# Optimization experiments

Hardware: AMD Instinct MI355X
Metric: run time of the kernel (lower is better)

## Reference

```python
import jax, jax.numpy as jnp
import numpy as np

B, NF, NI = 4, 8, 1
C_ASPP = 512
H32, W32 = 32, 32
H8, W8 = 128, 128
C = C_ASPP // 16  # 32 channels after PixelShuffle(4)
D = 32 * 4 + 4 * 1 + 4 + 1  # 137 dynamic-kernel params per instance
BN_EPS = 1e-5


def pixel_shuffle(x, r):
    # torch PixelShuffle: out[n, c, h*r+i, w*r+j] = in[n, c*r*r + i*r + j, h, w]
    n, cr2, h, w = x.shape
    c = cr2 // (r * r)
    x = x.reshape(n, c, r, r, h, w)
    x = x.transpose(0, 1, 4, 2, 5, 3)
    return x.reshape(n, c, h * r, w * r)


def conv2d(x, w, b, pad):
    y = jax.lax.conv_general_dilated(
        x, w, window_strides=(1, 1), padding=[(pad, pad), (pad, pad)],
        dimension_numbers=("NCHW", "OIHW", "NCHW"))
    return y + b[None, :, None, None]


def setup_inputs() -> dict:
    key = jax.random.key(0)
    ks = jax.random.split(key, 6)
    return {
        "embedding": jax.random.normal(ks[0], (B * NF, C_ASPP, H32, W32), jnp.float32),
        "inc_kernels": jax.random.normal(ks[1], (B, NF, NI, D), jnp.float32) * 0.1,
        "coarse_masks": jax.random.uniform(ks[2], (B, NF, NI, H8, W8), dtype=jnp.float32),
        "conv_w": jax.random.normal(ks[3], (C, C, 3, 3), jnp.float32) * 0.05,
        "conv_b": jnp.zeros((C,), jnp.float32),
        "bn_gamma": jnp.ones((C,), jnp.float32),
        "bn_beta": jnp.zeros((C,), jnp.float32),
        "bn_mean": jnp.zeros((C,), jnp.float32),
        "bn_var": jnp.ones((C,), jnp.float32),
        "smooth_w": jax.random.normal(ks[4], (1, 2, 5, 5), jnp.float32) * 0.05,
        "smooth_b": jnp.zeros((1,), jnp.float32),
    }


def reference(embedding, inc_kernels, coarse_masks, conv_w, conv_b,
              bn_gamma, bn_beta, bn_mean, bn_var, smooth_w, smooth_b):
    # inc_conv: PixelShuffle(4) -> Conv3x3 -> BatchNorm(eval) -> ReLU
    x = pixel_shuffle(embedding, 4)              # (B*NF, 32, 128, 128)
    x = conv2d(x, conv_w, conv_b, 1)
    scale = (bn_gamma / jnp.sqrt(bn_var + BN_EPS))[None, :, None, None]
    x = (x - bn_mean[None, :, None, None]) * scale + bn_beta[None, :, None, None]
    x = jax.nn.relu(x)

    # per-instance dynamic 1x1 convs (groups = B*NF*NI; NI=1 so each frame is a group)
    G = B * NF * NI
    k = inc_kernels.reshape(G, D)
    w1 = k[:, :128].reshape(G, 4, 32)            # layer1: 32 -> 4
    w2 = k[:, 128:132].reshape(G, 1, 4)          # layer2: 4 -> 1
    b1 = k[:, 132:136]
    b2 = k[:, 136:137]

    hfeat = jax.nn.relu(jnp.einsum('goc,gchw->gohw', w1, x) + b1[:, :, None, None])
    y = jnp.einsum('goc,gchw->gohw', w2, hfeat) + b2[:, :, None, None]  # (G,1,H8,W8)

    m = coarse_masks.reshape(G, 1, H8, W8)
    z = jnp.concatenate([jax.nn.sigmoid(y), m], axis=1)  # (G, 2, H8, W8)
    z = conv2d(z, smooth_w, smooth_b, 2)                 # inc_smooth 5x5
    return z.reshape(B * NF, NI, H8, W8)
```

## Files before the change

kernel.cpp:

```cpp
#include <hip/hip_runtime.h>


typedef __attribute__((ext_vector_type(8))) short short8;
typedef __attribute__((ext_vector_type(4))) float f32x4;

static __device__ __forceinline__ ushort f2bf(float x) {
    union { float f; uint u; } v; v.f = x;
    uint r = v.u + 0x7fffu + ((v.u >> 16) & 1u);
    return (ushort)(r >> 16);
}
static __device__ __forceinline__ float bf2f(ushort u) {
    union { uint u; float f; } v; v.u = ((uint)u) << 16; return v.f;
}

#define SIG_ELEMS (32 * 128 * 128)
#define BFRAG_OFF (SIG_ELEMS * 4)
#define SC_OFF    (BFRAG_OFF + 18432)
#define SH_OFF    (SC_OFF + 128)

__global__ void prep_kernel(const float* __restrict__ conv_w,
                            const float* __restrict__ conv_b,
                            const float* __restrict__ bn_gamma,
                            const float* __restrict__ bn_beta,
                            const float* __restrict__ bn_mean,
                            const float* __restrict__ bn_var,
                            ushort* __restrict__ bfrag,
                            float* __restrict__ scb, float* __restrict__ shb) {
    int t = blockIdx.x * 256 + threadIdx.x;
    if (t < 9216) {
        int j    = t & 7;
        int lane = (t >> 3) & 63;
        int knt  = t >> 9;
        int kk   = knt >> 1;
        int nt   = knt & 1;
        int oc   = (lane & 15) + nt * 16;
        int c    = (lane >> 4) * 8 + j;
        bfrag[t] = f2bf(conv_w[oc * 288 + c * 9 + kk]);
    } else if (t < 9248) {
        int oc = t - 9216;
        float sc = bn_gamma[oc] * rsqrtf(bn_var[oc] + 1e-5f);
        scb[oc] = sc;
        shb[oc] = (conv_b[oc] - bn_mean[oc]) * sc + bn_beta[oc];
    }
}

#define PITCHB 8320
#define BPITCH 258

__global__ __launch_bounds__(256, 4) void fused_main_kernel(
    const float* __restrict__ emb,
    const float* __restrict__ inc,
    const ushort* __restrict__ bfrag,
    const float* __restrict__ scb,
    const float* __restrict__ shb,
    float* __restrict__ sig_out)
{
    __shared__ __align__(16) char smem[4 * PITCHB];

    const int bid = blockIdx.x;
    const int lid = (bid & 7) * 256 + (bid >> 3);
    const int n    = lid >> 6;
    const int band = lid & 63;
    const int h0   = band << 1;

    const int tid  = threadIdx.x;
    const int lane = tid & 63;
    const int wv   = tid >> 6;
    const int g    = lane >> 4;
    const int m    = lane & 15;
    const int rw   = wv >> 1;
    const int xq   = (wv & 1) * 64;

    if (tid < 128) {
        int y   = tid >> 5;
        int col = (tid >> 4) & 1;
        int wrd = tid & 15;
        ((uint*)smem)[(y * PITCHB + (col ? 129 : 0) * 64) / 4 + wrd] = 0u;
    }

    #pragma unroll
    for (int k = 0; k < 8; ++k) {
        int u  = tid + (k << 8);
        int f  = u & 7;
        int sx = (u >> 3) & 3;
        int cp = (u >> 5) & 15;
        int y  = u >> 9;
        int h  = h0 + y - 1;
        float4 v0 = make_float4(0.f, 0.f, 0.f, 0.f);
        float4 v1 = v0;
        if ((unsigned)h < 128u) {
            int cc0  = cp * 32 + ((h & 3) << 2) + sx;
            long base = ((long)(n * 512 + cc0) << 10) + ((h >> 2) << 5) + (f << 2);
            v0 = *reinterpret_cast<const float4*>(&emb[base]);
            v1 = *reinterpret_cast<const float4*>(&emb[base + (16 << 10)]);
        }
        const float e0[4] = {v0.x, v0.y, v0.z, v0.w};
        const float e1[4] = {v1.x, v1.y, v1.z, v1.w};
        #pragma unroll
        for (int e = 0; e < 4; ++e) {
            int xi   = 1 + sx + (f << 4) + (e << 2);
            int slot = ((cp >> 2) ^ ((xi >> 1) ^ (xi >> 4))) & 3;
            uint pk  = ((uint)f2bf(e1[e]) << 16) | (uint)f2bf(e0[e]);
            ((uint*)smem)[(y * PITCHB + xi * 64 + (slot << 4) + ((cp & 3) << 2)) / 4] = pk;
        }
    }
    __syncthreads();

    int adr[4][3];
    #pragma unroll
    for (int t = 0; t < 4; ++t)
        #pragma unroll
        for (int dx = 0; dx < 3; ++dx) {
            int xi = xq + t * 16 + m + dx;
            int slot = (g ^ ((xi >> 1) ^ (xi >> 4))) & 3;
            adr[t][dx] = rw * PITCHB + xi * 64 + (slot << 4);
        }

    f32x4 acc[4][2];
    #pragma unroll
    for (int t = 0; t < 4; ++t)
        #pragma unroll
        for (int nt = 0; nt < 2; ++nt)
            acc[t][nt] = (f32x4){0.f, 0.f, 0.f, 0.f};

    #pragma unroll
    for (int kk = 0; kk < 9; ++kk) {
        const int dy = kk / 3, dxs = kk % 3;
        short8 b0 = *reinterpret_cast<const short8*>(bfrag + (((kk * 2 + 0) * 64 + lane) << 3));
        short8 b1 = *reinterpret_cast<const short8*>(bfrag + (((kk * 2 + 1) * 64 + lane) << 3));
        #pragma unroll
        for (int t = 0; t < 4; ++t) {
            short8 a = *reinterpret_cast<const short8*>(&smem[adr[t][dxs] + dy * PITCHB]);
            acc[t][0] = __builtin_amdgcn_mfma_f32_16x16x32_bf16(a, b0, acc[t][0], 0, 0, 0);
            acc[t][1] = __builtin_amdgcn_mfma_f32_16x16x32_bf16(a, b1, acc[t][1], 0, 0, 0);
        }
    }

    __syncthreads();
    {
        float sc0 = scb[m],      sh0 = shb[m];
        float sc1 = scb[m + 16], sh1 = shb[m + 16];
        uint* lb32 = (uint*)smem;
        #pragma unroll
        for (int t = 0; t < 4; ++t) {
            int pxb = rw * 128 + xq + t * 16 + g * 4;
            #pragma unroll
            for (int nt = 0; nt < 2; ++nt) {
                int oc = nt * 16 + m;
                float sc = nt ? sc1 : sc0, sh = nt ? sh1 : sh0;
                f32x4 A = acc[t][nt];
                float r0 = fmaxf(fmaf(A.x, sc, sh), 0.f);
                float r1 = fmaxf(fmaf(A.y, sc, sh), 0.f);
                float r2 = fmaxf(fmaf(A.z, sc, sh), 0.f);
                float r3 = fmaxf(fmaf(A.w, sc, sh), 0.f);
                int wbase = (oc * BPITCH + pxb) >> 1;
                lb32[wbase]     = ((uint)f2bf(r1) << 16) | (uint)f2bf(r0);
                lb32[wbase + 1] = ((uint)f2bf(r3) << 16) | (uint)f2bf(r2);
            }
        }
    }
    __syncthreads();

    {
        const ushort* lb = (const ushort*)smem;
        int px  = tid;
        int row = px >> 7, x = px & 127;
        float xv[32];
        #pragma unroll
        for (int c = 0; c < 32; ++c)
            xv[c] = bf2f(lb[c * BPITCH + px]);

        const float* hd = inc + n * 137;
        float y = hd[136];
        #pragma unroll
        for (int o = 0; o < 4; ++o) {
            float hv = hd[132 + o];
            #pragma unroll
            for (int c = 0; c < 32; ++c)
                hv = fmaf(hd[o * 32 + c], xv[c], hv);
            hv = fmaxf(hv, 0.0f);
            y = fmaf(hd[128 + o], hv, y);
        }
        float s = 1.0f / (1.0f + __expf(-y));
        sig_out[(n << 14) + ((h0 + row) << 7) + x] = s;
    }
}

__global__ __launch_bounds__(256) void smooth_kernel(
    const float* __restrict__ sig,
    const float* __restrict__ masks,
    const float* __restrict__ sw,
    const float* __restrict__ sb,
    float* __restrict__ out)
{
    __shared__ float ls[2][400];

    const int tid  = threadIdx.x;
    const int n    = blockIdx.x >> 6;
    const int tile = blockIdx.x & 63;
    const int h0   = (tile >> 3) << 4;
    const int w0   = (tile & 7) << 4;

    for (int i = tid; i < 800; i += 256) {
        int chn = (i >= 400) ? 1 : 0;
        int r  = i - chn * 400;
        int yy = r / 20;
        int xx = r - yy * 20;
        int h  = h0 + yy - 2;
        int w  = w0 + xx - 2;
        float v = 0.0f;
        if ((unsigned)h < 128u && (unsigned)w < 128u) {
            const float* src = chn ? masks : sig;
            v = src[(n << 14) + (h << 7) + w];
        }
        ls[chn][r] = v;
    }
    __syncthreads();

    const int tx = tid & 15;
    const int ty = tid >> 4;

    float accv = sb[0];
    #pragma unroll
    for (int chn = 0; chn < 2; ++chn)
        #pragma unroll
        for (int dy = 0; dy < 5; ++dy)
            #pragma unroll
            for (int dx = 0; dx < 5; ++dx)
                accv = fmaf(ls[chn][(ty + dy) * 20 + tx + dx],
                            sw[(chn * 5 + dy) * 5 + dx], accv);
    out[(n << 14) + ((h0 + ty) << 7) + (w0 + tx)] = accv;
}

extern "C" void kernel_launch(void* const* d_in, const int* in_sizes, int n_in,
                              void* d_out, int out_size, void* d_ws, size_t ws_size,
                              hipStream_t stream) {
    const float* emb     = (const float*)d_in[0];
    const float* inc     = (const float*)d_in[1];
    const float* masks   = (const float*)d_in[2];
    const float* conv_w  = (const float*)d_in[3];
    const float* conv_b  = (const float*)d_in[4];
    const float* bn_g    = (const float*)d_in[5];
    const float* bn_b    = (const float*)d_in[6];
    const float* bn_m    = (const float*)d_in[7];
    const float* bn_v    = (const float*)d_in[8];
    const float* sw      = (const float*)d_in[9];
    const float* sb      = (const float*)d_in[10];
    float*  out   = (float*)d_out;
    float*  sig   = (float*)d_ws;
    ushort* bfrag = (ushort*)((char*)d_ws + BFRAG_OFF);
    float*  scb   = (float*)((char*)d_ws + SC_OFF);
    float*  shb   = (float*)((char*)d_ws + SH_OFF);

    prep_kernel<<<37, 256, 0, stream>>>(conv_w, conv_b, bn_g, bn_b, bn_m, bn_v,
                                        bfrag, scb, shb);
    fused_main_kernel<<<2048, 256, 0, stream>>>(emb, inc, bfrag, scb, shb, sig);
    smooth_kernel<<<2048, 256, 0, stream>>>(sig, masks, sw, sb, out);
}
```

Before: 40.02 us.

## Batch input loads, use hardware bf16 pack, store activations as fp32 pixel-major

The staging loop now issues all eight pairs of global float4 loads before converting, and converts with the v_cvt_pk_bf16_f32 instruction instead of software rounding. The post-conv activation buffer switches from a bf16 channel-major layout to an fp32 pixel-major layout with a pitch of 36, so each thread reads its 32 channels as eight 16-byte vector loads. This removes the bf16 round-trip in the epilogue. In exchange, shared memory grows from about 33KB to about 36KB, which may limit occupancy at 4 blocks per CU, and the scattered per-element epilogue stores may cause bank conflicts.

After: 37.99 us. 1.05x faster.

```diff
diff --git a/kernel.cpp b/kernel.cpp
--- a/kernel.cpp
+++ b/kernel.cpp
@@ -9,8 +9,10 @@
     uint r = v.u + 0x7fffu + ((v.u >> 16) & 1u);
     return (ushort)(r >> 16);
 }
-static __device__ __forceinline__ float bf2f(ushort u) {
-    union { uint u; float f; } v; v.u = ((uint)u) << 16; return v.f;
+static __device__ __forceinline__ uint cvt_pk_bf16(float lo, float hi) {
+    uint r;
+    asm("v_cvt_pk_bf16_f32 %0, %1, %2" : "=v"(r) : "v"(lo), "v"(hi));
+    return r;
 }
 
 #define SIG_ELEMS (32 * 128 * 128)
@@ -45,7 +47,7 @@
 }
 
 #define PITCHB 8320
-#define BPITCH 258
+#define HPITCH 36
 
 __global__ __launch_bounds__(256, 4) void fused_main_kernel(
     const float* __restrict__ emb,
@@ -55,7 +57,7 @@
     const float* __restrict__ shb,
     float* __restrict__ sig_out)
 {
-    __shared__ __align__(16) char smem[4 * PITCHB];
+    __shared__ __align__(16) char smem[256 * HPITCH * 4];
 
     const int bid = blockIdx.x;
     const int lid = (bid & 7) * 256 + (bid >> 3);
@@ -78,6 +80,7 @@
         ((uint*)smem)[(y * PITCHB + (col ? 129 : 0) * 64) / 4 + wrd] = 0u;
     }
 
+    float4 pre0[8], pre1[8];
     #pragma unroll
     for (int k = 0; k < 8; ++k) {
         int u  = tid + (k << 8);
@@ -86,22 +89,32 @@
         int cp = (u >> 5) & 15;
         int y  = u >> 9;
         int h  = h0 + y - 1;
-        float4 v0 = make_float4(0.f, 0.f, 0.f, 0.f);
-        float4 v1 = v0;
+        pre0[k] = make_float4(0.f, 0.f, 0.f, 0.f);
+        pre1[k] = pre0[k];
         if ((unsigned)h < 128u) {
             int cc0  = cp * 32 + ((h & 3) << 2) + sx;
             long base = ((long)(n * 512 + cc0) << 10) + ((h >> 2) << 5) + (f << 2);
-            v0 = *reinterpret_cast<const float4*>(&emb[base]);
-            v1 = *reinterpret_cast<const float4*>(&emb[base + (16 << 10)]);
-        }
-        const float e0[4] = {v0.x, v0.y, v0.z, v0.w};
-        const float e1[4] = {v1.x, v1.y, v1.z, v1.w};
+            pre0[k] = *reinterpret_cast<const float4*>(&emb[base]);
+            pre1[k] = *reinterpret_cast<const float4*>(&emb[base + (16 << 10)]);
+        }
+    }
+    #pragma unroll
+    for (int k = 0; k < 8; ++k) {
+        int u  = tid + (k << 8);
+        int f  = u & 7;
+        int sx = (u >> 3) & 3;
+        int cp = (u >> 5) & 15;
+        int y  = u >> 9;
+        uint pk0 = cvt_pk_bf16(pre0[k].x, pre1[k].x);
+        uint pk1 = cvt_pk_bf16(pre0[k].y, pre1[k].y);
+        uint pk2 = cvt_pk_bf16(pre0[k].z, pre1[k].z);
+        uint pk3 = cvt_pk_bf16(pre0[k].w, pre1[k].w);
+        const uint pks[4] = {pk0, pk1, pk2, pk3};
         #pragma unroll
         for (int e = 0; e < 4; ++e) {
             int xi   = 1 + sx + (f << 4) + (e << 2);
             int slot = ((cp >> 2) ^ ((xi >> 1) ^ (xi >> 4))) & 3;
-            uint pk  = ((uint)f2bf(e1[e]) << 16) | (uint)f2bf(e0[e]);
-            ((uint*)smem)[(y * PITCHB + xi * 64 + (slot << 4) + ((cp & 3) << 2)) / 4] = pk;
+            ((uint*)smem)[(y * PITCHB + xi * 64 + (slot << 4) + ((cp & 3) << 2)) / 4] = pks[e];
         }
     }
     __syncthreads();
@@ -138,9 +151,9 @@
 
     __syncthreads();
     {
+        float* lb = (float*)smem;
         float sc0 = scb[m],      sh0 = shb[m];
         float sc1 = scb[m + 16], sh1 = shb[m + 16];
-        uint* lb32 = (uint*)smem;
         #pragma unroll
         for (int t = 0; t < 4; ++t) {
             int pxb = rw * 128 + xq + t * 16 + g * 4;
@@ -149,26 +162,20 @@
                 int oc = nt * 16 + m;
                 float sc = nt ? sc1 : sc0, sh = nt ? sh1 : sh0;
                 f32x4 A = acc[t][nt];
-                float r0 = fmaxf(fmaf(A.x, sc, sh), 0.f);
-                float r1 = fmaxf(fmaf(A.y, sc, sh), 0.f);
-                float r2 = fmaxf(fmaf(A.z, sc, sh), 0.f);
-                float r3 = fmaxf(fmaf(A.w, sc, sh), 0.f);
-                int wbase = (oc * BPITCH + pxb) >> 1;
-                lb32[wbase]     = ((uint)f2bf(r1) << 16) | (uint)f2bf(r0);
-                lb32[wbase + 1] = ((uint)f2bf(r3) << 16) | (uint)f2bf(r2);
+                lb[(pxb + 0) * HPITCH + oc] = fmaxf(fmaf(A.x, sc, sh), 0.f);
+                lb[(pxb + 1) * HPITCH + oc] = fmaxf(fmaf(A.y, sc, sh), 0.f);
+                lb[(pxb + 2) * HPITCH + oc] = fmaxf(fmaf(A.z, sc, sh), 0.f);
+                lb[(pxb + 3) * HPITCH + oc] = fmaxf(fmaf(A.w, sc, sh), 0.f);
             }
         }
     }
     __syncthreads();
 
     {
-        const ushort* lb = (const ushort*)smem;
-        int px  = tid;
-        int row = px >> 7, x = px & 127;
-        float xv[32];
-        #pragma unroll
-        for (int c = 0; c < 32; ++c)
-            xv[c] = bf2f(lb[c * BPITCH + px]);
+        const f32x4* row = reinterpret_cast<const f32x4*>((float*)smem + tid * HPITCH);
+        f32x4 xv[8];
+        #pragma unroll
+        for (int q = 0; q < 8; ++q) xv[q] = row[q];
 
         const float* hd = inc + n * 137;
         float y = hd[136];
@@ -176,13 +183,18 @@
         for (int o = 0; o < 4; ++o) {
             float hv = hd[132 + o];
             #pragma unroll
-            for (int c = 0; c < 32; ++c)
-                hv = fmaf(hd[o * 32 + c], xv[c], hv);
+            for (int q = 0; q < 8; ++q) {
+                hv = fmaf(hd[o * 32 + q * 4 + 0], xv[q].x, hv);
+                hv = fmaf(hd[o * 32 + q * 4 + 1], xv[q].y, hv);
+                hv = fmaf(hd[o * 32 + q * 4 + 2], xv[q].z, hv);
+                hv = fmaf(hd[o * 32 + q * 4 + 3], xv[q].w, hv);
+            }
             hv = fmaxf(hv, 0.0f);
             y = fmaf(hd[128 + o], hv, y);
         }
         float s = 1.0f / (1.0f + __expf(-y));
-        sig_out[(n << 14) + ((h0 + row) << 7) + x] = s;
+        int row_i = tid >> 7, x = tid & 127;
+        sig_out[(n << 14) + ((h0 + row_i) << 7) + x] = s;
     }
 }
 
```

## Fuse BN-ReLU and dynamic 1x1 convs into MFMA epilogue, batch embedding loads

Applied to the files above, without the earlier changes.

The BN scale is folded into the bf16 conv weights, and the MFMA operands are swapped so each lane holds output channels for one pixel. This lets the BN shift, ReLU and per-instance 1x1 convs run directly on the accumulators, with cross-lane shuffle reductions replacing the LDS round-trip and two extra barriers. The embedding staging issues all global loads up front before any LDS writes, packs pairs with v_cvt_pk_bf16 and uses 16-byte LDS stores. Dynamic kernel params are padded to a 144 stride for vector loads, which adds work to the prep kernel and keeps more values live in registers.

After: 36.61 us. 8.5% less time.

```diff
diff --git a/kernel.cpp b/kernel.cpp
--- a/kernel.cpp
+++ b/kernel.cpp
@@ -9,14 +9,16 @@
     uint r = v.u + 0x7fffu + ((v.u >> 16) & 1u);
     return (ushort)(r >> 16);
 }
-static __device__ __forceinline__ float bf2f(ushort u) {
-    union { uint u; float f; } v; v.u = ((uint)u) << 16; return v.f;
+static __device__ __forceinline__ uint cvt_pk_bf16(float lo, float hi) {
+    uint r;
+    asm("v_cvt_pk_bf16_f32 %0, %1, %2" : "=v"(r) : "v"(lo), "v"(hi));
+    return r;
 }
 
 #define SIG_ELEMS (32 * 128 * 128)
 #define BFRAG_OFF (SIG_ELEMS * 4)
-#define SC_OFF    (BFRAG_OFF + 18432)
-#define SH_OFF    (SC_OFF + 128)
+#define SH_OFF    (BFRAG_OFF + 18432)
+#define HDP_OFF   (SH_OFF + 128)
 
 __global__ void prep_kernel(const float* __restrict__ conv_w,
                             const float* __restrict__ conv_b,
@@ -24,8 +26,10 @@
                             const float* __restrict__ bn_beta,
                             const float* __restrict__ bn_mean,
                             const float* __restrict__ bn_var,
+                            const float* __restrict__ inc,
                             ushort* __restrict__ bfrag,
-                            float* __restrict__ scb, float* __restrict__ shb) {
+                            float* __restrict__ shb,
+                            float* __restrict__ hdp) {
     int t = blockIdx.x * 256 + threadIdx.x;
     if (t < 9216) {
         int j    = t & 7;
@@ -35,24 +39,26 @@
         int nt   = knt & 1;
         int oc   = (lane & 15) + nt * 16;
         int c    = (lane >> 4) * 8 + j;
-        bfrag[t] = f2bf(conv_w[oc * 288 + c * 9 + kk]);
+        float sc = bn_gamma[oc] * rsqrtf(bn_var[oc] + 1e-5f);
+        bfrag[t] = f2bf(conv_w[oc * 288 + c * 9 + kk] * sc);
     } else if (t < 9248) {
         int oc = t - 9216;
         float sc = bn_gamma[oc] * rsqrtf(bn_var[oc] + 1e-5f);
-        scb[oc] = sc;
         shb[oc] = (conv_b[oc] - bn_mean[oc]) * sc + bn_beta[oc];
+    } else if (t < 9248 + 32 * 137) {
+        int i = t - 9248;
+        int nn = i / 137, r = i - nn * 137;
+        hdp[nn * 144 + r] = inc[i];
     }
 }
 
 #define PITCHB 8320
-#define BPITCH 258
 
 __global__ __launch_bounds__(256, 4) void fused_main_kernel(
     const float* __restrict__ emb,
-    const float* __restrict__ inc,
     const ushort* __restrict__ bfrag,
-    const float* __restrict__ scb,
     const float* __restrict__ shb,
+    const float* __restrict__ hdp,
     float* __restrict__ sig_out)
 {
     __shared__ __align__(16) char smem[4 * PITCHB];
@@ -64,6 +70,80 @@
     const int h0   = band << 1;
 
     const int tid  = threadIdx.x;
+
+    const int f    = tid & 7;
+    const int cphi = (tid >> 3) & 3;
+    const int sx   = (tid >> 5) & 3;
+    const int yA   = tid >> 7;
+    const int yB   = yA + 2;
+    const int hA   = h0 + yA - 1;
+    const int hB   = h0 + yB - 1;
+    const bool vA  = (unsigned)hA < 128u;
+    const bool vB  = (unsigned)hB < 128u;
+
+    float4 pA0[4], pA1[4], pB0[4], pB1[4];
+    #pragma unroll
+    for (int cplo = 0; cplo < 4; ++cplo) {
+        pA0[cplo] = make_float4(0.f, 0.f, 0.f, 0.f);
+        pA1[cplo] = pA0[cplo]; pB0[cplo] = pA0[cplo]; pB1[cplo] = pA0[cplo];
+        if (vA) {
+            int cc = cphi * 128 + cplo * 32 + ((hA & 3) << 2) + sx;
+            long base = ((long)(n * 512 + cc) << 10) + ((hA >> 2) << 5) + (f << 2);
+            pA0[cplo] = *reinterpret_cast<const float4*>(&emb[base]);
+            pA1[cplo] = *reinterpret_cast<const float4*>(&emb[base + (16 << 10)]);
+        }
+        if (vB) {
+            int cc = cphi * 128 + cplo * 32 + ((hB & 3) << 2) + sx;
+            long base = ((long)(n * 512 + cc) << 10) + ((hB >> 2) << 5) + (f << 2);
+            pB0[cplo] = *reinterpret_cast<const float4*>(&emb[base]);
+            pB1[cplo] = *reinterpret_cast<const float4*>(&emb[base + (16 << 10)]);
+        }
+    }
+    __builtin_amdgcn_sched_barrier(0);
+
+    if (tid < 128) {
+        int y   = tid >> 5;
+        int col = (tid >> 4) & 1;
+        int wrd = tid & 15;
+        ((uint*)smem)[(y * PITCHB + (col ? 129 : 0) * 64) / 4 + wrd] = 0u;
+    }
+
+    #pragma unroll
+    for (int e = 0; e < 4; ++e) {
+        int xi   = 1 + sx + (f << 4) + (e << 2);
+        int slot = (cphi ^ ((xi >> 1) ^ (xi >> 4))) & 3;
+        int off  = xi * 64 + (slot << 4);
+        const float a00[4] = {pA0[0].x, pA0[0].y, pA0[0].z, pA0[0].w};
+        const float a01[4] = {pA0[1].x, pA0[1].y, pA0[1].z, pA0[1].w};
+        const float a02[4] = {pA0[2].x, pA0[2].y, pA0[2].z, pA0[2].w};
+        const float a03[4] = {pA0[3].x, pA0[3].y, pA0[3].z, pA0[3].w};
+        const float a10[4] = {pA1[0].x, pA1[0].y, pA1[0].z, pA1[0].w};
+        const float a11[4] = {pA1[1].x, pA1[1].y, pA1[1].z, pA1[1].w};
+        const float a12[4] = {pA1[2].x, pA1[2].y, pA1[2].z, pA1[2].w};
+        const float a13[4] = {pA1[3].x, pA1[3].y, pA1[3].z, pA1[3].w};
+        uint4 qa;
+        qa.x = cvt_pk_bf16(a00[e], a10[e]);
+        qa.y = cvt_pk_bf16(a01[e], a11[e]);
+        qa.z = cvt_pk_bf16(a02[e], a12[e]);
+        qa.w = cvt_pk_bf16(a03[e], a13[e]);
+        *reinterpret_cast<uint4*>(&smem[yA * PITCHB + off]) = qa;
+        const float b00[4] = {pB0[0].x, pB0[0].y, pB0[0].z, pB0[0].w};
+        const float b01[4] = {pB0[1].x, pB0[1].y, pB0[1].z, pB0[1].w};
+        const float b02[4] = {pB0[2].x, pB0[2].y, pB0[2].z, pB0[2].w};
+        const float b03[4] = {pB0[3].x, pB0[3].y, pB0[3].z, pB0[3].w};
+        const float b10[4] = {pB1[0].x, pB1[0].y, pB1[0].z, pB1[0].w};
+        const float b11[4] = {pB1[1].x, pB1[1].y, pB1[1].z, pB1[1].w};
+        const float b12[4] = {pB1[2].x, pB1[2].y, pB1[2].z, pB1[2].w};
+        const float b13[4] = {pB1[3].x, pB1[3].y, pB1[3].z, pB1[3].w};
+        uint4 qb;
+        qb.x = cvt_pk_bf16(b00[e], b10[e]);
+        qb.y = cvt_pk_bf16(b01[e], b11[e]);
+        qb.z = cvt_pk_bf16(b02[e], b12[e]);
+        qb.w = cvt_pk_bf16(b03[e], b13[e]);
+        *reinterpret_cast<uint4*>(&smem[yB * PITCHB + off]) = qb;
+    }
+    __syncthreads();
+
     const int lane = tid & 63;
     const int wv   = tid >> 6;
     const int g    = lane >> 4;
@@ -71,41 +151,6 @@
     const int rw   = wv >> 1;
     const int xq   = (wv & 1) * 64;
 
-    if (tid < 128) {
-        int y   = tid >> 5;
-        int col = (tid >> 4) & 1;
-        int wrd = tid & 15;
-        ((uint*)smem)[(y * PITCHB + (col ? 129 : 0) * 64) / 4 + wrd] = 0u;
-    }
-
-    #pragma unroll
-    for (int k = 0; k < 8; ++k) {
-        int u  = tid + (k << 8);
-        int f  = u & 7;
-        int sx = (u >> 3) & 3;
-        int cp = (u >> 5) & 15;
-        int y  = u >> 9;
-        int h  = h0 + y - 1;
-        float4 v0 = make_float4(0.f, 0.f, 0.f, 0.f);
-        float4 v1 = v0;
-        if ((unsigned)h < 128u) {
-            int cc0  = cp * 32 + ((h & 3) << 2) + sx;
-            long base = ((long)(n * 512 + cc0) << 10) + ((h >> 2) << 5) + (f << 2);
-            v0 = *reinterpret_cast<const float4*>(&emb[base]);
-            v1 = *reinterpret_cast<const float4*>(&emb[base + (16 << 10)]);
-        }
-        const float e0[4] = {v0.x, v0.y, v0.z, v0.w};
-        const float e1[4] = {v1.x, v1.y, v1.z, v1.w};
-        #pragma unroll
-        for (int e = 0; e < 4; ++e) {
-            int xi   = 1 + sx + (f << 4) + (e << 2);
-            int slot = ((cp >> 2) ^ ((xi >> 1) ^ (xi >> 4))) & 3;
-            uint pk  = ((uint)f2bf(e1[e]) << 16) | (uint)f2bf(e0[e]);
-            ((uint*)smem)[(y * PITCHB + xi * 64 + (slot << 4) + ((cp & 3) << 2)) / 4] = pk;
-        }
-    }
-    __syncthreads();
-
     int adr[4][3];
     #pragma unroll
     for (int t = 0; t < 4; ++t)
@@ -131,59 +176,76 @@
         #pragma unroll
         for (int t = 0; t < 4; ++t) {
             short8 a = *reinterpret_cast<const short8*>(&smem[adr[t][dxs] + dy * PITCHB]);
-            acc[t][0] = __builtin_amdgcn_mfma_f32_16x16x32_bf16(a, b0, acc[t][0], 0, 0, 0);
-            acc[t][1] = __builtin_amdgcn_mfma_f32_16x16x32_bf16(a, b1, acc[t][1], 0, 0, 0);
-        }
-    }
-
-    __syncthreads();
-    {
-        float sc0 = scb[m],      sh0 = shb[m];
-        float sc1 = scb[m + 16], sh1 = shb[m + 16];
-        uint* lb32 = (uint*)smem;
-        #pragma unroll
-        for (int t = 0; t < 4; ++t) {
-            int pxb = rw * 128 + xq + t * 16 + g * 4;
-            #pragma unroll
-            for (int nt = 0; nt < 2; ++nt) {
-                int oc = nt * 16 + m;
-                float sc = nt ? sc1 : sc0, sh = nt ? sh1 : sh0;
-                f32x4 A = acc[t][nt];
-                float r0 = fmaxf(fmaf(A.x, sc, sh), 0.f);
-                float r1 = fmaxf(fmaf(A.y, sc, sh), 0.f);
-                float r2 = fmaxf(fmaf(A.z, sc, sh), 0.f);
-                float r3 = fmaxf(fmaf(A.w, sc, sh), 0.f);
-                int wbase = (oc * BPITCH + pxb) >> 1;
-                lb32[wbase]     = ((uint)f2bf(r1) << 16) | (uint)f2bf(r0);
-                lb32[wbase + 1] = ((uint)f2bf(r3) << 16) | (uint)f2bf(r2);
-            }
-        }
-    }
-    __syncthreads();
-
-    {
-        const ushort* lb = (const ushort*)smem;
-        int px  = tid;
-        int row = px >> 7, x = px & 127;
-        float xv[32];
-        #pragma unroll
-        for (int c = 0; c < 32; ++c)
-            xv[c] = bf2f(lb[c * BPITCH + px]);
-
-        const float* hd = inc + n * 137;
-        float y = hd[136];
+            acc[t][0] = __builtin_amdgcn_mfma_f32_16x16x32_bf16(b0, a, acc[t][0], 0, 0, 0);
+            acc[t][1] = __builtin_amdgcn_mfma_f32_16x16x32_bf16(b1, a, acc[t][1], 0, 0, 0);
+        }
+    }
+
+    const float* hd = hdp + n * 144;
+    const f32x4 shA = *reinterpret_cast<const f32x4*>(&shb[g * 4]);
+    const f32x4 shB = *reinterpret_cast<const f32x4*>(&shb[16 + g * 4]);
+    f32x4 w1A[4], w1B[4];
+    #pragma unroll
+    for (int o = 0; o < 4; ++o) {
+        w1A[o] = *reinterpret_cast<const f32x4*>(&hd[o * 32 + g * 4]);
+        w1B[o] = *reinterpret_cast<const f32x4*>(&hd[o * 32 + 16 + g * 4]);
+    }
+
+    float ph[4][4];
+    #pragma unroll
+    for (int t = 0; t < 4; ++t) {
+        f32x4 vA, vB;
+        vA.x = fmaxf(acc[t][0].x + shA.x, 0.f);
+        vA.y = fmaxf(acc[t][0].y + shA.y, 0.f);
+        vA.z = fmaxf(acc[t][0].z + shA.z, 0.f);
+        vA.w = fmaxf(acc[t][0].w + shA.w, 0.f);
+        vB.x = fmaxf(acc[t][1].x + shB.x, 0.f);
+        vB.y = fmaxf(acc[t][1].y + shB.y, 0.f);
+        vB.z = fmaxf(acc[t][1].z + shB.z, 0.f);
+        vB.w = fmaxf(acc[t][1].w + shB.w, 0.f);
         #pragma unroll
         for (int o = 0; o < 4; ++o) {
-            float hv = hd[132 + o];
-            #pragma unroll
-            for (int c = 0; c < 32; ++c)
-                hv = fmaf(hd[o * 32 + c], xv[c], hv);
-            hv = fmaxf(hv, 0.0f);
-            y = fmaf(hd[128 + o], hv, y);
-        }
-        float s = 1.0f / (1.0f + __expf(-y));
-        sig_out[(n << 14) + ((h0 + row) << 7) + x] = s;
-    }
+            float p = vA.x * w1A[o].x;
+            p = fmaf(vA.y, w1A[o].y, p);
+            p = fmaf(vA.z, w1A[o].z, p);
+            p = fmaf(vA.w, w1A[o].w, p);
+            p = fmaf(vB.x, w1B[o].x, p);
+            p = fmaf(vB.y, w1B[o].y, p);
+            p = fmaf(vB.z, w1B[o].z, p);
+            p = fmaf(vB.w, w1B[o].w, p);
+            ph[t][o] = p;
+        }
+    }
+    #pragma unroll
+    for (int t = 0; t < 4; ++t)
+        #pragma unroll
+        for (int o = 0; o < 4; ++o) {
+            float s = ph[t][o];
+            s += __shfl_xor(s, 16);
+            s += __shfl_xor(s, 32);
+            ph[t][o] = s;
+        }
+
+    const f32x4 w2v = *reinterpret_cast<const f32x4*>(&hd[128]);
+    const f32x4 b1v = *reinterpret_cast<const f32x4*>(&hd[132]);
+    const float b2  = hd[136];
+    float yv[4];
+    #pragma unroll
+    for (int t = 0; t < 4; ++t) {
+        float q0 = fmaxf(ph[t][0] + b1v.x, 0.f);
+        float q1 = fmaxf(ph[t][1] + b1v.y, 0.f);
+        float q2 = fmaxf(ph[t][2] + b1v.z, 0.f);
+        float q3 = fmaxf(ph[t][3] + b1v.w, 0.f);
+        float yy = b2;
+        yy = fmaf(w2v.x, q0, yy);
+        yy = fmaf(w2v.y, q1, yy);
+        yy = fmaf(w2v.z, q2, yy);
+        yy = fmaf(w2v.w, q3, yy);
+        yv[t] = yy;
+    }
+    float ysel = (g == 0) ? yv[0] : (g == 1) ? yv[1] : (g == 2) ? yv[2] : yv[3];
+    float s = 1.0f / (1.0f + __expf(-ysel));
+    sig_out[(n << 14) + ((h0 + rw) << 7) + xq + lane] = s;
 }
 
 __global__ __launch_bounds__(256) void smooth_kernel(
@@ -249,11 +311,11 @@
     float*  out   = (float*)d_out;
     float*  sig   = (float*)d_ws;
     ushort* bfrag = (ushort*)((char*)d_ws + BFRAG_OFF);
-    float*  scb   = (float*)((char*)d_ws + SC_OFF);
     float*  shb   = (float*)((char*)d_ws + SH_OFF);
-
-    prep_kernel<<<37, 256, 0, stream>>>(conv_w, conv_b, bn_g, bn_b, bn_m, bn_v,
-                                        bfrag, scb, shb);
-    fused_main_kernel<<<2048, 256, 0, stream>>>(emb, inc, bfrag, scb, shb, sig);
+    float*  hdp   = (float*)((char*)d_ws + HDP_OFF);
+
+    prep_kernel<<<54, 256, 0, stream>>>(conv_w, conv_b, bn_g, bn_b, bn_m, bn_v,
+                                        inc, bfrag, shb, hdp);
+    fused_main_kernel<<<2048, 256, 0, stream>>>(emb, bfrag, shb, hdp, sig);
     smooth_kernel<<<2048, 256, 0, stream>>>(sig, masks, sw, sb, out);
 }
```
